# Kernel tuning notes

Measured on AMD Instinct MI355X. Metric: run time of the kernel, lower is better.

Reference implementation:

```python
import jax, jax.numpy as jnp
import numpy as np

N = 35        # brain ROIs, hardcoded by x.repeat(35,1,1)
NV = 6        # number of views (edge_attr feature dim)
C1, C2, C3 = 256, 256, 128  # conv channel widths (scaled-up config.PARAMS)
E = N * N     # fully connected graph incl. self loops (helper.cast_data)


def setup_inputs() -> dict:
    key = jax.random.key(0)
    ks = jax.random.split(key, 16)

    def lin(k, fin, fout):
        return jax.random.normal(k, (fin, fout), jnp.float32) / np.sqrt(fin)

    src = jnp.repeat(jnp.arange(N, dtype=jnp.int32), N)
    dst = jnp.tile(jnp.arange(N, dtype=jnp.int32), N)
    return {
        "x": jnp.ones((N, 1), jnp.float32),
        "edge_attr": jax.random.uniform(ks[0], (E, NV), jnp.float32),
        "edge_index": jnp.stack([src, dst]),
        # edge-conditioned MLP weights (Linear(NV, cin*cout) + ReLU)
        "nn1_w": lin(ks[1], NV, 1 * C1),  "nn1_b": jnp.zeros((1 * C1,), jnp.float32),
        "nn2_w": lin(ks[2], NV, C1 * C2), "nn2_b": jnp.zeros((C1 * C2,), jnp.float32),
        "nn3_w": lin(ks[3], NV, C2 * C3), "nn3_b": jnp.zeros((C2 * C3,), jnp.float32),
        # NNConv root weights + biases (PyG defaults)
        "root1": lin(ks[4], 1, C1),  "bias1": jnp.zeros((C1,), jnp.float32),
        "root2": lin(ks[5], C1, C2), "bias2": jnp.zeros((C2,), jnp.float32),
        "root3": lin(ks[6], C2, C3), "bias3": jnp.zeros((C3,), jnp.float32),
    }


def _nnconv(x, edge_attr, src, dst, nn_w, nn_b, root, bias, cin, cout):
    # per-edge weight matrix from edge features: [E, cin, cout]
    W = jax.nn.relu(edge_attr @ nn_w + nn_b).reshape(-1, cin, cout)
    # gather source node feats, per-edge matvec: [E, cout]
    msg = jnp.einsum('ei,eio->eo', x[src], W)
    # scatter-mean into targets
    s = jax.ops.segment_sum(msg, dst, num_segments=N)
    cnt = jax.ops.segment_sum(jnp.ones(msg.shape[0], msg.dtype), dst, num_segments=N)
    agg = s / jnp.maximum(cnt, 1.0)[:, None]
    return agg + x @ root + bias


def reference(x, edge_attr, edge_index, nn1_w, nn1_b, nn2_w, nn2_b, nn3_w, nn3_b,
              root1, bias1, root2, bias2, root3, bias3):
    src, dst = edge_index[0], edge_index[1]
    h = jax.nn.relu(_nnconv(x, edge_attr, src, dst, nn1_w, nn1_b, root1, bias1, 1, C1))
    h = jax.nn.relu(_nnconv(h, edge_attr, src, dst, nn2_w, nn2_b, root2, bias2, C1, C2))
    h = jax.nn.relu(_nnconv(h, edge_attr, src, dst, nn3_w, nn3_b, root3, bias3, C2, C3))
    # cbt[i, j] = sum_f |h[j, f] - h[i, f]|  (x.repeat/transpose/abs/sum)
    cbt = jnp.sum(jnp.abs(h[None, :, :] - h[:, None, :]), axis=2)
    return cbt
```

## Files before the change

### kernel.cpp

```cpp
#include <hip/hip_runtime.h>

#define N  35
#define E  (N*N)
#define C1 256
#define C2 256
#define C3 128


__global__ __launch_bounds__(C1) void k_layer1(
    const float* __restrict__ x, const float* __restrict__ ea,
    const float* __restrict__ nn1w, const float* __restrict__ nn1b,
    const float* __restrict__ root1, const float* __restrict__ bias1,
    float* __restrict__ h1, float* __restrict__ aggz)
{
    for (int t = blockIdx.x * blockDim.x + threadIdx.x; t < 8960 + 4480;
         t += gridDim.x * blockDim.x)
        aggz[t] = 0.f;

    int j = blockIdx.x;
    int o = threadIdx.x;
    float w[6];
#pragma unroll
    for (int v = 0; v < 6; ++v) w[v] = nn1w[v * C1 + o];
    float b = nn1b[o];
    float acc = 0.f;
    for (int i = 0; i < N; ++i) {
        int e = i * N + j;
        float p = b;
#pragma unroll
        for (int v = 0; v < 6; ++v) p = fmaf(ea[e * 6 + v], w[v], p);
        p = fmaxf(p, 0.f);
        acc = fmaf(x[i], p, acc);
    }
    float s = acc * (1.f / N) + x[j] * root1[o] + bias1[o];
    h1[j * C1 + o] = fmaxf(s, 0.f);
}

__global__ __launch_bounds__(256) void k_l2(
    const float* __restrict__ ea,
    const float* __restrict__ w2, const float* __restrict__ b2,
    const float* __restrict__ h1, const float* __restrict__ root2,
    float* __restrict__ agg2)
{
    const int j     = blockIdx.x % N;
    const int chunk = blockIdx.x / N;
    const int o     = threadIdx.x;

    if (chunk < 32) {
        const int c0 = chunk * 8;
        __shared__ float ea_s[N * 6];
        __shared__ float h1_s[N * 8];
        if (o < N * 6) { int i = o / 6, v = o % 6; ea_s[o] = ea[(i * N + j) * 6 + v]; }
        for (int t = o; t < N * 8; t += 256) {
            int i = t >> 3, cc = t & 7;
            h1_s[t] = h1[i * C1 + c0 + cc];
        }
        __syncthreads();

        float wv[8][6], bb[8], acc[8];
#pragma unroll
        for (int cc = 0; cc < 8; ++cc) {
            int col = (c0 + cc) * C2 + o;
#pragma unroll
            for (int v = 0; v < 6; ++v) wv[cc][v] = w2[v * (C1 * C2) + col];
            bb[cc] = b2[col];
            acc[cc] = 0.f;
        }
#pragma unroll 5
        for (int i = 0; i < N; ++i) {
            const float2 e01 = *(const float2*)&ea_s[i * 6];
            const float2 e23 = *(const float2*)&ea_s[i * 6 + 2];
            const float2 e45 = *(const float2*)&ea_s[i * 6 + 4];
            const float4 ha  = *(const float4*)&h1_s[i * 8];
            const float4 hb  = *(const float4*)&h1_s[i * 8 + 4];
            const float hv[8] = {ha.x, ha.y, ha.z, ha.w, hb.x, hb.y, hb.z, hb.w};
#pragma unroll
            for (int cc = 0; cc < 8; ++cc) {
                float p = fmaf(e01.x, wv[cc][0], bb[cc]);
                p = fmaf(e01.y, wv[cc][1], p);
                p = fmaf(e23.x, wv[cc][2], p);
                p = fmaf(e23.y, wv[cc][3], p);
                p = fmaf(e45.x, wv[cc][4], p);
                p = fmaf(e45.y, wv[cc][5], p);
                p = fmaxf(p, 0.f);
                acc[cc] = fmaf(hv[cc], p, acc[cc]);
            }
        }
        float s = 0.f;
#pragma unroll
        for (int cc = 0; cc < 8; ++cc) s += acc[cc];
        atomicAdd(&agg2[j * C2 + o], s * (1.f / N));
    } else {
        const int c0 = (chunk - 32) * 32;
        float s = 0.f;
#pragma unroll 8
        for (int c = c0; c < c0 + 32; ++c)
            s = fmaf(h1[j * C1 + c], root2[c * C2 + o], s);
        atomicAdd(&agg2[j * C2 + o], s);
    }
}

__global__ __launch_bounds__(256) void k_l3(
    const float* __restrict__ ea,
    const float* __restrict__ w3, const float* __restrict__ b3,
    const float* __restrict__ agg2, const float* __restrict__ bias2,
    const float* __restrict__ root3,
    float* __restrict__ agg3)
{
    const int j     = blockIdx.x % N;
    const int chunk = blockIdx.x / N;
    const int tid   = threadIdx.x;
    const int o     = tid & (C3 - 1);
    const int half  = tid >> 7;

    if (chunk < 32) {
        const int c0 = chunk * 8;
        __shared__ float ea_s[N * 6];
        __shared__ float h2_s[N * 8];
        if (tid < N * 6) { int i = tid / 6, v = tid % 6; ea_s[tid] = ea[(i * N + j) * 6 + v]; }
        for (int t = tid; t < N * 8; t += 256) {
            int i = t >> 3, cc = t & 7;
            int c = c0 + cc;
            h2_s[t] = fmaxf(agg2[i * C2 + c] + bias2[c], 0.f);
        }
        __syncthreads();

        float wv[8][6], bb[8], acc[8];
#pragma unroll
        for (int cc = 0; cc < 8; ++cc) {
            int col = (c0 + cc) * C3 + o;
#pragma unroll
            for (int v = 0; v < 6; ++v) wv[cc][v] = w3[v * (C2 * C3) + col];
            bb[cc] = b3[col];
            acc[cc] = 0.f;
        }
        const int ibeg = half ? 18 : 0;
        const int iend = half ? N  : 18;
        for (int i = ibeg; i < iend; ++i) {
            const float2 e01 = *(const float2*)&ea_s[i * 6];
            const float2 e23 = *(const float2*)&ea_s[i * 6 + 2];
            const float2 e45 = *(const float2*)&ea_s[i * 6 + 4];
            const float4 ha  = *(const float4*)&h2_s[i * 8];
            const float4 hb  = *(const float4*)&h2_s[i * 8 + 4];
            const float hv[8] = {ha.x, ha.y, ha.z, ha.w, hb.x, hb.y, hb.z, hb.w};
#pragma unroll
            for (int cc = 0; cc < 8; ++cc) {
                float p = fmaf(e01.x, wv[cc][0], bb[cc]);
                p = fmaf(e01.y, wv[cc][1], p);
                p = fmaf(e23.x, wv[cc][2], p);
                p = fmaf(e23.y, wv[cc][3], p);
                p = fmaf(e45.x, wv[cc][4], p);
                p = fmaf(e45.y, wv[cc][5], p);
                p = fmaxf(p, 0.f);
                acc[cc] = fmaf(hv[cc], p, acc[cc]);
            }
        }
        float s = 0.f;
#pragma unroll
        for (int cc = 0; cc < 8; ++cc) s += acc[cc];
        atomicAdd(&agg3[j * C3 + o], s * (1.f / N));
    } else {
        const int c0 = (chunk - 32) * 64 + half * 32;
        float s = 0.f;
#pragma unroll 8
        for (int c = c0; c < c0 + 32; ++c) {
            float hv = fmaxf(agg2[j * C2 + c] + bias2[c], 0.f);
            s = fmaf(hv, root3[c * C3 + o], s);
        }
        atomicAdd(&agg3[j * C3 + o], s);
    }
}

__global__ __launch_bounds__(256) void k_cbt(
    const float* __restrict__ agg3, const float* __restrict__ bias3,
    float* __restrict__ out)
{
    int t = blockIdx.x * 256 + threadIdx.x;
    if (t >= E) return;
    int i = t / N, j = t % N;
    float acc = 0.f;
#pragma unroll
    for (int f = 0; f < C3 / 4; ++f) {
        float4 a  = *(const float4*)&agg3[i * C3 + f * 4];
        float4 b  = *(const float4*)&agg3[j * C3 + f * 4];
        float4 bi = *(const float4*)&bias3[f * 4];
        float ax = fmaxf(a.x + bi.x, 0.f), bx = fmaxf(b.x + bi.x, 0.f);
        float ay = fmaxf(a.y + bi.y, 0.f), by = fmaxf(b.y + bi.y, 0.f);
        float az = fmaxf(a.z + bi.z, 0.f), bz = fmaxf(b.z + bi.z, 0.f);
        float aw = fmaxf(a.w + bi.w, 0.f), bw = fmaxf(b.w + bi.w, 0.f);
        acc += fabsf(bx - ax) + fabsf(by - ay) + fabsf(bz - az) + fabsf(bw - aw);
    }
    out[t] = acc;
}

extern "C" void kernel_launch(void* const* d_in, const int* in_sizes, int n_in,
                              void* d_out, int out_size, void* d_ws, size_t ws_size,
                              hipStream_t stream)
{
    const float* x     = (const float*)d_in[0];
    const float* ea    = (const float*)d_in[1];
    const float* nn1w  = (const float*)d_in[3];
    const float* nn1b  = (const float*)d_in[4];
    const float* nn2w  = (const float*)d_in[5];
    const float* nn2b  = (const float*)d_in[6];
    const float* nn3w  = (const float*)d_in[7];
    const float* nn3b  = (const float*)d_in[8];
    const float* root1 = (const float*)d_in[9];
    const float* bias1 = (const float*)d_in[10];
    const float* root2 = (const float*)d_in[11];
    const float* bias2 = (const float*)d_in[12];
    const float* root3 = (const float*)d_in[13];
    const float* bias3 = (const float*)d_in[14];

    float* ws   = (float*)d_ws;
    float* h1   = ws;
    float* agg2 = ws + 8960;
    float* agg3 = ws + 8960 + 8960;

    k_layer1<<<N, C1, 0, stream>>>(x, ea, nn1w, nn1b, root1, bias1, h1, agg2);
    k_l2<<<N * 40, 256, 0, stream>>>(ea, nn2w, nn2b, h1, root2, agg2);
    k_l3<<<N * 36, 256, 0, stream>>>(ea, nn3w, nn3b, agg2, bias2, root3, agg3);
    k_cbt<<<(E + 255) / 256, 256, 0, stream>>>(agg3, bias3, (float*)d_out);
}
```

Before: 43.74 us.

## Split layer2/3 edge-MLP work into 4-channel chunks and stage cbt features in LDS

Layers 2 and 3 now process 4 input channels per block instead of 8, doubling the grid (N*72 and N*68 blocks) so more blocks are spread across the GPU, with less register pressure but more atomicAdd traffic. Edge attributes are staged in LDS padded to 8 floats so one float4 plus one float2 load fetch a row. Layer 1 also stages edge attributes in LDS and zeroes the accumulators with float4 stores. The cbt kernel preloads ReLU'd layer-3 features into padded LDS so global reloads and the repeated bias/ReLU work go away.

```diff
diff --git a/kernel.cpp b/kernel.cpp
--- a/kernel.cpp
+++ b/kernel.cpp
@@ -13,24 +13,37 @@
     const float* __restrict__ root1, const float* __restrict__ bias1,
     float* __restrict__ h1, float* __restrict__ aggz)
 {
-    for (int t = blockIdx.x * blockDim.x + threadIdx.x; t < 8960 + 4480;
-         t += gridDim.x * blockDim.x)
-        aggz[t] = 0.f;
-
-    int j = blockIdx.x;
-    int o = threadIdx.x;
+    const int j = blockIdx.x;
+    const int o = threadIdx.x;
+
+    {
+        int t = blockIdx.x * C1 + threadIdx.x;
+        if (t < 3360) {
+            float4 z; z.x = z.y = z.z = z.w = 0.f;
+            ((float4*)aggz)[t] = z;
+        }
+    }
+
+    __shared__ float ea_s[N * 8];
+    if (o < N * 6) { int i = o / 6, v = o % 6; ea_s[i * 8 + v] = ea[(i * N + j) * 6 + v]; }
+    __syncthreads();
+
     float w[6];
 #pragma unroll
     for (int v = 0; v < 6; ++v) w[v] = nn1w[v * C1 + o];
-    float b = nn1b[o];
+    const float b = nn1b[o];
     float acc = 0.f;
+#pragma unroll 7
     for (int i = 0; i < N; ++i) {
-        int e = i * N + j;
-        float p = b;
-#pragma unroll
-        for (int v = 0; v < 6; ++v) p = fmaf(ea[e * 6 + v], w[v], p);
-        p = fmaxf(p, 0.f);
-        acc = fmaf(x[i], p, acc);
+        const float4 ef = *(const float4*)&ea_s[i * 8];
+        const float2 eg = *(const float2*)&ea_s[i * 8 + 4];
+        float p = fmaf(ef.x, w[0], b);
+        p = fmaf(ef.y, w[1], p);
+        p = fmaf(ef.z, w[2], p);
+        p = fmaf(ef.w, w[3], p);
+        p = fmaf(eg.x, w[4], p);
+        p = fmaf(eg.y, w[5], p);
+        acc = fmaf(x[i], fmaxf(p, 0.f), acc);
     }
     float s = acc * (1.f / N) + x[j] * root1[o] + bias1[o];
     h1[j * C1 + o] = fmaxf(s, 0.f);
@@ -46,52 +59,45 @@
     const int chunk = blockIdx.x / N;
     const int o     = threadIdx.x;
 
-    if (chunk < 32) {
-        const int c0 = chunk * 8;
-        __shared__ float ea_s[N * 6];
-        __shared__ float h1_s[N * 8];
-        if (o < N * 6) { int i = o / 6, v = o % 6; ea_s[o] = ea[(i * N + j) * 6 + v]; }
-        for (int t = o; t < N * 8; t += 256) {
-            int i = t >> 3, cc = t & 7;
-            h1_s[t] = h1[i * C1 + c0 + cc];
-        }
+    if (chunk < 64) {
+        const int c0 = chunk * 4;
+        __shared__ float ea_s[N * 8];
+        __shared__ float h_s[N * 4];
+        if (o < N * 6) { int i = o / 6, v = o % 6; ea_s[i * 8 + v] = ea[(i * N + j) * 6 + v]; }
+        if (o < N * 4) { int i = o >> 2, cc = o & 3; h_s[o] = h1[i * C1 + c0 + cc]; }
         __syncthreads();
 
-        float wv[8][6], bb[8], acc[8];
-#pragma unroll
-        for (int cc = 0; cc < 8; ++cc) {
+        float wv[4][6], bb[4], acc[4];
+#pragma unroll
+        for (int cc = 0; cc < 4; ++cc) {
             int col = (c0 + cc) * C2 + o;
 #pragma unroll
             for (int v = 0; v < 6; ++v) wv[cc][v] = w2[v * (C1 * C2) + col];
             bb[cc] = b2[col];
             acc[cc] = 0.f;
         }
-#pragma unroll 5
+#pragma unroll 7
         for (int i = 0; i < N; ++i) {
-            const float2 e01 = *(const float2*)&ea_s[i * 6];
-            const float2 e23 = *(const float2*)&ea_s[i * 6 + 2];
-            const float2 e45 = *(const float2*)&ea_s[i * 6 + 4];
-            const float4 ha  = *(const float4*)&h1_s[i * 8];
-            const float4 hb  = *(const float4*)&h1_s[i * 8 + 4];
-            const float hv[8] = {ha.x, ha.y, ha.z, ha.w, hb.x, hb.y, hb.z, hb.w};
-#pragma unroll
-            for (int cc = 0; cc < 8; ++cc) {
-                float p = fmaf(e01.x, wv[cc][0], bb[cc]);
-                p = fmaf(e01.y, wv[cc][1], p);
-                p = fmaf(e23.x, wv[cc][2], p);
-                p = fmaf(e23.y, wv[cc][3], p);
-                p = fmaf(e45.x, wv[cc][4], p);
-                p = fmaf(e45.y, wv[cc][5], p);
+            const float4 ef = *(const float4*)&ea_s[i * 8];
+            const float2 eg = *(const float2*)&ea_s[i * 8 + 4];
+            const float4 h4 = *(const float4*)&h_s[i * 4];
+            const float hv[4] = {h4.x, h4.y, h4.z, h4.w};
+#pragma unroll
+            for (int cc = 0; cc < 4; ++cc) {
+                float p = fmaf(ef.x, wv[cc][0], bb[cc]);
+                p = fmaf(ef.y, wv[cc][1], p);
+                p = fmaf(ef.z, wv[cc][2], p);
+                p = fmaf(ef.w, wv[cc][3], p);
+                p = fmaf(eg.x, wv[cc][4], p);
+                p = fmaf(eg.y, wv[cc][5], p);
                 p = fmaxf(p, 0.f);
                 acc[cc] = fmaf(hv[cc], p, acc[cc]);
             }
         }
-        float s = 0.f;
-#pragma unroll
-        for (int cc = 0; cc < 8; ++cc) s += acc[cc];
+        float s = (acc[0] + acc[1]) + (acc[2] + acc[3]);
         atomicAdd(&agg2[j * C2 + o], s * (1.f / N));
     } else {
-        const int c0 = (chunk - 32) * 32;
+        const int c0 = (chunk - 64) * 32;
         float s = 0.f;
 #pragma unroll 8
         for (int c = c0; c < c0 + 32; ++c)
@@ -113,21 +119,21 @@
     const int o     = tid & (C3 - 1);
     const int half  = tid >> 7;
 
-    if (chunk < 32) {
-        const int c0 = chunk * 8;
-        __shared__ float ea_s[N * 6];
-        __shared__ float h2_s[N * 8];
-        if (tid < N * 6) { int i = tid / 6, v = tid % 6; ea_s[tid] = ea[(i * N + j) * 6 + v]; }
-        for (int t = tid; t < N * 8; t += 256) {
-            int i = t >> 3, cc = t & 7;
+    if (chunk < 64) {
+        const int c0 = chunk * 4;
+        __shared__ float ea_s[N * 8];
+        __shared__ float h2_s[N * 4];
+        if (tid < N * 6) { int i = tid / 6, v = tid % 6; ea_s[i * 8 + v] = ea[(i * N + j) * 6 + v]; }
+        if (tid < N * 4) {
+            int i = tid >> 2, cc = tid & 3;
             int c = c0 + cc;
-            h2_s[t] = fmaxf(agg2[i * C2 + c] + bias2[c], 0.f);
+            h2_s[tid] = fmaxf(agg2[i * C2 + c] + bias2[c], 0.f);
         }
         __syncthreads();
 
-        float wv[8][6], bb[8], acc[8];
-#pragma unroll
-        for (int cc = 0; cc < 8; ++cc) {
+        float wv[4][6], bb[4], acc[4];
+#pragma unroll
+        for (int cc = 0; cc < 4; ++cc) {
             int col = (c0 + cc) * C3 + o;
 #pragma unroll
             for (int v = 0; v < 6; ++v) wv[cc][v] = w3[v * (C2 * C3) + col];
@@ -137,30 +143,26 @@
         const int ibeg = half ? 18 : 0;
         const int iend = half ? N  : 18;
         for (int i = ibeg; i < iend; ++i) {
-            const float2 e01 = *(const float2*)&ea_s[i * 6];
-            const float2 e23 = *(const float2*)&ea_s[i * 6 + 2];
-            const float2 e45 = *(const float2*)&ea_s[i * 6 + 4];
-            const float4 ha  = *(const float4*)&h2_s[i * 8];
-            const float4 hb  = *(const float4*)&h2_s[i * 8 + 4];
-            const float hv[8] = {ha.x, ha.y, ha.z, ha.w, hb.x, hb.y, hb.z, hb.w};
-#pragma unroll
-            for (int cc = 0; cc < 8; ++cc) {
-                float p = fmaf(e01.x, wv[cc][0], bb[cc]);
-                p = fmaf(e01.y, wv[cc][1], p);
-                p = fmaf(e23.x, wv[cc][2], p);
-                p = fmaf(e23.y, wv[cc][3], p);
-                p = fmaf(e45.x, wv[cc][4], p);
-                p = fmaf(e45.y, wv[cc][5], p);
+            const float4 ef = *(const float4*)&ea_s[i * 8];
+            const float2 eg = *(const float2*)&ea_s[i * 8 + 4];
+            const float4 h4 = *(const float4*)&h2_s[i * 4];
+            const float hv[4] = {h4.x, h4.y, h4.z, h4.w};
+#pragma unroll
+            for (int cc = 0; cc < 4; ++cc) {
+                float p = fmaf(ef.x, wv[cc][0], bb[cc]);
+                p = fmaf(ef.y, wv[cc][1], p);
+                p = fmaf(ef.z, wv[cc][2], p);
+                p = fmaf(ef.w, wv[cc][3], p);
+                p = fmaf(eg.x, wv[cc][4], p);
+                p = fmaf(eg.y, wv[cc][5], p);
                 p = fmaxf(p, 0.f);
                 acc[cc] = fmaf(hv[cc], p, acc[cc]);
             }
         }
-        float s = 0.f;
-#pragma unroll
-        for (int cc = 0; cc < 8; ++cc) s += acc[cc];
+        float s = (acc[0] + acc[1]) + (acc[2] + acc[3]);
         atomicAdd(&agg3[j * C3 + o], s * (1.f / N));
     } else {
-        const int c0 = (chunk - 32) * 64 + half * 32;
+        const int c0 = (chunk - 64) * 64 + half * 32;
         float s = 0.f;
 #pragma unroll 8
         for (int c = c0; c < c0 + 32; ++c) {
@@ -171,24 +173,30 @@
     }
 }
 
+#define H3PAD 132
 __global__ __launch_bounds__(256) void k_cbt(
     const float* __restrict__ agg3, const float* __restrict__ bias3,
     float* __restrict__ out)
 {
-    int t = blockIdx.x * 256 + threadIdx.x;
+    __shared__ float h3s[N * H3PAD];
+    const int tid = threadIdx.x;
+    for (int t = tid; t < N * C3; t += 256) {
+        int i = t >> 7, f = t & (C3 - 1);
+        h3s[i * H3PAD + f] = fmaxf(agg3[t] + bias3[f], 0.f);
+    }
+    __syncthreads();
+
+    int t = blockIdx.x * 256 + tid;
     if (t >= E) return;
     int i = t / N, j = t % N;
+    const float* hi = &h3s[i * H3PAD];
+    const float* hj = &h3s[j * H3PAD];
     float acc = 0.f;
 #pragma unroll
     for (int f = 0; f < C3 / 4; ++f) {
-        float4 a  = *(const float4*)&agg3[i * C3 + f * 4];
-        float4 b  = *(const float4*)&agg3[j * C3 + f * 4];
-        float4 bi = *(const float4*)&bias3[f * 4];
-        float ax = fmaxf(a.x + bi.x, 0.f), bx = fmaxf(b.x + bi.x, 0.f);
-        float ay = fmaxf(a.y + bi.y, 0.f), by = fmaxf(b.y + bi.y, 0.f);
-        float az = fmaxf(a.z + bi.z, 0.f), bz = fmaxf(b.z + bi.z, 0.f);
-        float aw = fmaxf(a.w + bi.w, 0.f), bw = fmaxf(b.w + bi.w, 0.f);
-        acc += fabsf(bx - ax) + fabsf(by - ay) + fabsf(bz - az) + fabsf(bw - aw);
+        float4 a = *(const float4*)&hi[f * 4];
+        float4 b = *(const float4*)&hj[f * 4];
+        acc += fabsf(b.x - a.x) + fabsf(b.y - a.y) + fabsf(b.z - a.z) + fabsf(b.w - a.w);
     }
     out[t] = acc;
 }
@@ -218,7 +226,7 @@
     float* agg3 = ws + 8960 + 8960;
 
     k_layer1<<<N, C1, 0, stream>>>(x, ea, nn1w, nn1b, root1, bias1, h1, agg2);
-    k_l2<<<N * 40, 256, 0, stream>>>(ea, nn2w, nn2b, h1, root2, agg2);
-    k_l3<<<N * 36, 256, 0, stream>>>(ea, nn3w, nn3b, agg2, bias2, root3, agg3);
+    k_l2<<<N * 72, 256, 0, stream>>>(ea, nn2w, nn2b, h1, root2, agg2);
+    k_l3<<<N * 68, 256, 0, stream>>>(ea, nn3w, nn3b, agg2, bias2, root3, agg3);
     k_cbt<<<(E + 255) / 256, 256, 0, stream>>>(agg3, bias3, (float*)d_out);
 }
```

After: 36.70 us, median of 2. 1.19x faster.
